# Kernel optimization log

Measured on AMD Instinct MI355X. Metric: run time of the kernel, lower is better.

Reference implementation:

```python
import jax, jax.numpy as jnp
import numpy as np

N = 50000      # nodes (full graph: num_dst == num_src == N)
E = 800000     # edges, avg degree 16
D = 128        # in_feats == n_hidden == out_feats
L = 3          # n_layers
EPS = 1e-5     # BatchNorm1d eps


def setup_inputs() -> dict:
    key = jax.random.key(0)
    ks = jax.random.split(key, 6)
    feat = jax.random.normal(ks[0], (N, D), dtype=jnp.float32)
    src = jax.random.randint(ks[1], (E,), 0, N)
    dst = jax.random.randint(ks[2], (E,), 0, N)
    scale = 1.0 / np.sqrt(D)
    W_self = jax.random.normal(ks[3], (L, D, D), dtype=jnp.float32) * scale
    W_neigh = jax.random.normal(ks[4], (L, D, D), dtype=jnp.float32) * scale
    b = jax.random.normal(ks[5], (L, D), dtype=jnp.float32) * 0.01
    gamma = jnp.ones((L - 1, D), dtype=jnp.float32)
    beta = jnp.zeros((L - 1, D), dtype=jnp.float32)
    return {"feat": feat, "src": src, "dst": dst, "W_self": W_self,
            "W_neigh": W_neigh, "b": b, "gamma": gamma, "beta": beta}


def reference(feat, src, dst, W_self, W_neigh, b, gamma, beta):
    n = feat.shape[0]
    n_layers = W_self.shape[0]
    # in-degree of each dst node, clamped to 1 (zero-degree nodes aggregate 0)
    deg = jax.ops.segment_sum(jnp.ones_like(dst, dtype=feat.dtype), dst,
                              num_segments=n)
    deg = jnp.maximum(deg, 1.0)[:, None]                      # [N,1]
    h = feat
    for i in range(n_layers):
        # mean aggregation over incoming neighbors: gather + segment-sum
        agg = jax.ops.segment_sum(h[src], dst, num_segments=n) / deg  # [N,D]
        # SAGEConv('mean'): fc_self(h_dst) + fc_neigh(agg) + bias
        hn = h @ W_self[i] + agg @ W_neigh[i] + b[i]
        hn = hn + h                                           # residual (dims match)
        if i < n_layers - 1:
            mu = jnp.mean(hn, axis=0)
            var = jnp.var(hn, axis=0)                         # biased, as BN training
            hn = (hn - mu) * jax.lax.rsqrt(var + EPS) * gamma[i] + beta[i]
            hn = jax.nn.relu(hn)
        h = hn
    return h
```

## Files before the change

kernel.cpp:

```cpp
#include <hip/hip_runtime.h>

#define DIM 128
#define EPSF 1e-5f
#define BK_SHIFT 10
#define BK_NODES 1024
#define BK_CAP 20480

typedef __attribute__((ext_vector_type(8))) short short8;
typedef __attribute__((ext_vector_type(8))) unsigned short ushort8;
typedef __attribute__((ext_vector_type(4))) float float4v;

__device__ inline unsigned short f2bf(float x) {
    union { float f; unsigned u; } z; z.f = x;
    unsigned u = z.u;
    unsigned r = u + 0x7FFF + ((u >> 16) & 1);
    return (unsigned short)(r >> 16);
}
__device__ inline float bf2f(unsigned short u) {
    union { unsigned u; float f; } z; z.u = ((unsigned)u) << 16;
    return z.f;
}

__global__ void binA_kernel(const int* __restrict__ src, const int* __restrict__ dst,
                            unsigned* __restrict__ barr, int* __restrict__ bcnt,
                            int E, int NB) {
    __shared__ int cnt[64];
    __shared__ int gcur[64];
    int tid = threadIdx.x;
    int tile0 = blockIdx.x * 4096;
    if (tid < 64) cnt[tid] = 0;
    __syncthreads();
    unsigned pk[16]; int bk[16];
#pragma unroll
    for (int i = 0; i < 16; ++i) {
        int e = tile0 + i * 256 + tid;
        if (e < E) {
            int d = dst[e];
            int s = src[e];
            bk[i] = d >> BK_SHIFT;
            pk[i] = ((unsigned)(d & (BK_NODES - 1)) << 16) | (unsigned)s;
            atomicAdd(&cnt[bk[i]], 1);
        } else bk[i] = -1;
    }
    __syncthreads();
    if (tid < 64) {
        int c = (tid < NB) ? cnt[tid] : 0;
        gcur[tid] = (c > 0) ? atomicAdd(&bcnt[tid], c) : 0;
    }
    __syncthreads();
#pragma unroll
    for (int i = 0; i < 16; ++i) {
        if (bk[i] >= 0) {
            int pos = atomicAdd(&gcur[bk[i]], 1);
            if (pos < BK_CAP)
                barr[(size_t)bk[i] * BK_CAP + pos] = pk[i];
        }
    }
}

__global__ void bucketscan_kernel(const int* __restrict__ bcnt, int* __restrict__ bbase,
                                  int NB, int* __restrict__ rowptr, int N, int E) {
    if (threadIdx.x == 0) {
        int run = 0;
        for (int b = 0; b < NB; ++b) { bbase[b] = run; run += bcnt[b]; }
        rowptr[N] = E;
    }
}

__global__ void binB_kernel(const unsigned* __restrict__ barr, const int* __restrict__ bcnt,
                            const int* __restrict__ bbase, int* __restrict__ rowptr,
                            int* __restrict__ colidx, int N) {
    __shared__ int hist[BK_NODES];
    __shared__ int sm[256];
    int b = blockIdx.x;
    int tid = threadIdx.x;
    int cnt = bcnt[b];
    if (cnt > BK_CAP) cnt = BK_CAP;
    const unsigned* arr = barr + (size_t)b * BK_CAP;
    int gb = bbase[b];
#pragma unroll
    for (int j = 0; j < 4; ++j) hist[tid * 4 + j] = 0;
    __syncthreads();
    for (int i = tid; i < cnt; i += 256)
        atomicAdd(&hist[arr[i] >> 16], 1);
    __syncthreads();
    int h[4], s = 0;
#pragma unroll
    for (int j = 0; j < 4; ++j) { h[j] = hist[tid * 4 + j]; s += h[j]; }
    sm[tid] = s;
    __syncthreads();
    int tot = s;
    for (int off = 1; off < 256; off <<= 1) {
        int x = (tid >= off) ? sm[tid - off] : 0;
        __syncthreads();
        sm[tid] += x;
        __syncthreads();
    }
    int run = sm[tid] - tot;
#pragma unroll
    for (int j = 0; j < 4; ++j) { hist[tid * 4 + j] = run; run += h[j]; }
    __syncthreads();
    int nbase = b << BK_SHIFT;
    int nn = N - nbase; if (nn > BK_NODES) nn = BK_NODES;
    for (int j = tid; j < nn; j += 256)
        rowptr[nbase + j] = gb + hist[j];
    __syncthreads();
    for (int i = tid; i < cnt; i += 256) {
        unsigned u = arr[i];
        int pos = atomicAdd(&hist[u >> 16], 1);
        colidx[gb + pos] = (int)(u & 0xFFFFu);
    }
}

__global__ void packw_kernel(const float* __restrict__ Ws, const float* __restrict__ Wn,
                             unsigned short* __restrict__ wpack) {
    int l = blockIdx.x >> 3;
    int s = blockIdx.x & 7;
    int tid = threadIdx.x;
#pragma unroll
    for (int pi = 0; pi < 2; ++pi) {
        int p = tid * 2 + pi;
        int nt = p >> 6;
        int lane = p & 63;
        int kb = s * 32 + (lane >> 4) * 8;
        int col = nt * 16 + (lane & 15);
        unsigned short* dstp = wpack + (size_t)l * 32768 + ((size_t)(s * 8 + nt) * 64 + lane) * 8;
#pragma unroll
        for (int j = 0; j < 8; ++j) {
            int k = kb + j;
            float v = (k < 128) ? Ws[(size_t)l * 16384 + k * 128 + col]
                                : Wn[(size_t)l * 16384 + (k - 128) * 128 + col];
            dstp[j] = f2bf(v);
        }
    }
}

__global__ void convert_kernel(const float* __restrict__ feat, unsigned short* __restrict__ Acat,
                               int N) {
    int idx = blockIdx.x * blockDim.x + threadIdx.x;
    if (idx >= N * 32) return;
    float4 v = ((const float4*)feat)[idx];
    int r = idx >> 5, c4 = idx & 31;
    ushort4 o;
    o.x = f2bf(v.x); o.y = f2bf(v.y); o.z = f2bf(v.z); o.w = f2bf(v.w);
    ((ushort4*)Acat)[(size_t)r * 64 + c4] = o;
}

__global__ void aggregate_kernel(unsigned short* Acat, const int* __restrict__ rowptr,
                                 const int* __restrict__ colidx, int N) {
    int wid = (blockIdx.x * blockDim.x + threadIdx.x) >> 6;
    if (wid >= N) return;
    int lane = threadIdx.x & 63;
    int half = lane >> 5, sl = lane & 31;
    int beg = rowptr[wid], end = rowptr[wid + 1];
    float4 acc = make_float4(0.f, 0.f, 0.f, 0.f);
    int e = beg + half;
    for (; e + 2 < end; e += 4) {
        int s0 = colidx[e];
        int s1 = colidx[e + 2];
        ushort4 u0 = *(const ushort4*)(Acat + (size_t)s0 * 256 + sl * 4);
        ushort4 u1 = *(const ushort4*)(Acat + (size_t)s1 * 256 + sl * 4);
        acc.x += bf2f(u0.x) + bf2f(u1.x);
        acc.y += bf2f(u0.y) + bf2f(u1.y);
        acc.z += bf2f(u0.z) + bf2f(u1.z);
        acc.w += bf2f(u0.w) + bf2f(u1.w);
    }
    if (e < end) {
        int s0 = colidx[e];
        ushort4 u0 = *(const ushort4*)(Acat + (size_t)s0 * 256 + sl * 4);
        acc.x += bf2f(u0.x);
        acc.y += bf2f(u0.y);
        acc.z += bf2f(u0.z);
        acc.w += bf2f(u0.w);
    }
    acc.x += __shfl_xor(acc.x, 32);
    acc.y += __shfl_xor(acc.y, 32);
    acc.z += __shfl_xor(acc.z, 32);
    acc.w += __shfl_xor(acc.w, 32);
    if (half == 0) {
        int deg = end - beg;
        float inv = 1.0f / (float)(deg > 0 ? deg : 1);
        ushort4 o;
        o.x = f2bf(acc.x * inv); o.y = f2bf(acc.y * inv);
        o.z = f2bf(acc.z * inv); o.w = f2bf(acc.w * inv);
        *(ushort4*)(Acat + (size_t)wid * 256 + 128 + sl * 4) = o;
    }
}

__launch_bounds__(256)
__global__ void gemm_kernel(const unsigned short* __restrict__ Acat,
                            const unsigned short* __restrict__ wpack,
                            const float* __restrict__ bias,
                            unsigned short* __restrict__ outb, float* __restrict__ outf,
                            float* __restrict__ stats, int withStats, int N) {
    __shared__ unsigned short Bs[32768];
    int tid = threadIdx.x;
    {
        const float4* wsrc = (const float4*)wpack;
        float4* bdst = (float4*)Bs;
#pragma unroll
        for (int i = 0; i < 16; ++i) bdst[i * 256 + tid] = wsrc[i * 256 + tid];
    }
    __syncthreads();

    int wave = tid >> 6, lane = tid & 63;
    int row0 = blockIdx.x * 128 + wave * 32;
    int mrow = lane & 15, kq = lane >> 4;
    const unsigned short* Abase = Acat + (size_t)(row0 + mrow) * 256 + kq * 8;

    float4v acc[2][8];
#pragma unroll
    for (int i = 0; i < 2; ++i)
#pragma unroll
        for (int j = 0; j < 8; ++j) acc[i][j] = (float4v){0.f, 0.f, 0.f, 0.f};

#pragma unroll
    for (int s = 0; s < 8; ++s) {
        short8 a0 = *(const short8*)(Abase + s * 32);
        short8 a1 = *(const short8*)(Abase + 16 * 256 + s * 32);
#pragma unroll
        for (int nt = 0; nt < 8; ++nt) {
            short8 b = *(const short8*)(Bs + ((size_t)(s * 8 + nt) * 64 + lane) * 8);
            acc[0][nt] = __builtin_amdgcn_mfma_f32_16x16x32_bf16(a0, b, acc[0][nt], 0, 0, 0);
            acc[1][nt] = __builtin_amdgcn_mfma_f32_16x16x32_bf16(a1, b, acc[1][nt], 0, 0, 0);
        }
    }

    float* sm = (float*)Bs;
    if (withStats) {
        __syncthreads();
        sm[tid] = 0.f;
        __syncthreads();
    }

    int colb = lane & 15;
    int rq = (lane >> 4) * 4;
#pragma unroll
    for (int mt = 0; mt < 2; ++mt) {
        int rowt = row0 + mt * 16 + rq;
#pragma unroll
        for (int nt = 0; nt < 8; ++nt) {
            int col = nt * 16 + colb;
            float bv = bias[col];
            float slo = 0.f, qlo = 0.f;
#pragma unroll
            for (int r = 0; r < 4; ++r) {
                int row = rowt + r;
                if (row < N) {
                    float res = bf2f(Acat[(size_t)row * 256 + col]);
                    float v = acc[mt][nt][r] + bv + res;
                    if (withStats) {
                        outb[(size_t)row * 128 + col] = f2bf(v);
                        slo += v; qlo += v * v;
                    } else {
                        outf[(size_t)row * 128 + col] = v;
                    }
                }
            }
            if (withStats) {
                atomicAdd(&sm[col], slo);
                atomicAdd(&sm[128 + col], qlo);
            }
        }
    }
    if (withStats) {
        __syncthreads();
        if (tid < 128) {
            atomicAdd(&stats[tid], sm[tid]);
            atomicAdd(&stats[128 + tid], sm[128 + tid]);
        }
    }
}

__global__ void bnapply_kernel(const unsigned short* __restrict__ hn,
                               unsigned short* __restrict__ Acat,
                               const float* __restrict__ stats, const float* __restrict__ gamma,
                               const float* __restrict__ beta, float invN, int N) {
    __shared__ float sc_s[128], sh_s[128];
    int tid = threadIdx.x;
    if (tid < 128) {
        float mean = stats[tid] * invN;
        float var = stats[128 + tid] * invN - mean * mean;
        float sc = gamma[tid] * rsqrtf(var + EPSF);
        sc_s[tid] = sc;
        sh_s[tid] = beta[tid] - mean * sc;
    }
    __syncthreads();
    int idx = blockIdx.x * 256 + tid;
    if (idx >= N * 32) return;
    int row = idx >> 5, c4 = idx & 31;
    ushort4 u = *(const ushort4*)(hn + (size_t)idx * 4);
    ushort4 o;
    {
        int col = c4 * 4;
        float v0 = fmaf(bf2f(u.x), sc_s[col], sh_s[col]);
        float v1 = fmaf(bf2f(u.y), sc_s[col + 1], sh_s[col + 1]);
        float v2 = fmaf(bf2f(u.z), sc_s[col + 2], sh_s[col + 2]);
        float v3 = fmaf(bf2f(u.w), sc_s[col + 3], sh_s[col + 3]);
        o.x = f2bf(fmaxf(v0, 0.f));
        o.y = f2bf(fmaxf(v1, 0.f));
        o.z = f2bf(fmaxf(v2, 0.f));
        o.w = f2bf(fmaxf(v3, 0.f));
    }
    *(ushort4*)(Acat + (size_t)row * 256 + c4 * 4) = o;
}

extern "C" void kernel_launch(void* const* d_in, const int* in_sizes, int n_in,
                              void* d_out, int out_size, void* d_ws, size_t ws_size,
                              hipStream_t stream) {
    const float* feat  = (const float*)d_in[0];
    const int*   src   = (const int*)d_in[1];
    const int*   dst   = (const int*)d_in[2];
    const float* Wself = (const float*)d_in[3];
    const float* Wneig = (const float*)d_in[4];
    const float* bias  = (const float*)d_in[5];
    const float* gamma = (const float*)d_in[6];
    const float* beta  = (const float*)d_in[7];

    int N = in_sizes[0] / DIM;
    int E = in_sizes[1];
    int Npad = (N + 127) & ~127;
    int NB = (N + BK_NODES - 1) >> BK_SHIFT;

    char* ws = (char*)d_ws;
    size_t off = 0;
    auto alloc = [&](size_t bytes) -> void* {
        void* p = ws + off;
        off = (off + bytes + 255) & ~(size_t)255;
        return p;
    };
    unsigned short* Acat   = (unsigned short*)alloc((size_t)Npad * 256 * 2);
    unsigned short* hnS    = (unsigned short*)alloc((size_t)Npad * 128 * 2);
    unsigned short* wpack  = (unsigned short*)alloc((size_t)3 * 32768 * 2);
    int*   colidx = (int*)alloc((size_t)E * 4);
    int*   rowptr = (int*)alloc((size_t)(N + 1) * 4);
    int*   bcnt   = (int*)alloc(64 * 4);
    int*   bbase  = (int*)alloc(64 * 4);
    float* stats  = (float*)alloc(256 * 4);

    unsigned* barr = (unsigned*)Acat;

    hipMemsetAsync(bcnt, 0, 64 * 4, stream);
    binA_kernel<<<(E + 4095) / 4096, 256, 0, stream>>>(src, dst, barr, bcnt, E, NB);
    bucketscan_kernel<<<1, 64, 0, stream>>>(bcnt, bbase, NB, rowptr, N, E);
    binB_kernel<<<NB, 256, 0, stream>>>(barr, bcnt, bbase, rowptr, colidx, N);

    packw_kernel<<<24, 256, 0, stream>>>(Wself, Wneig, wpack);
    convert_kernel<<<(N * 32 + 255) / 256, 256, 0, stream>>>(feat, Acat, N);
    if (Npad > N)
        hipMemsetAsync(Acat + (size_t)N * 256, 0, (size_t)(Npad - N) * 512, stream);

    float invN = 1.0f / (float)N;

    for (int l = 0; l < 3; ++l) {
        aggregate_kernel<<<(N + 3) / 4, 256, 0, stream>>>(Acat, rowptr, colidx, N);
        int withStats = (l < 2) ? 1 : 0;
        if (withStats) hipMemsetAsync(stats, 0, 256 * 4, stream);
        gemm_kernel<<<Npad / 128, 256, 0, stream>>>(
            Acat, wpack + (size_t)l * 32768, bias + (size_t)l * DIM,
            hnS, (float*)d_out, stats, withStats, N);
        if (withStats)
            bnapply_kernel<<<(N * 32 + 255) / 256, 256, 0, stream>>>(
                hnS, Acat, stats, gamma + (size_t)l * DIM, beta + (size_t)l * DIM, invN, N);
    }
}
```

Baseline: 364.5 us.

## Fold bucket scan into binB, zero stats in aggregate, use half-wave per node

Removes the single-thread bucketscan launch by having each binB block compute its own prefix from the bucket counts in shared memory. Removes the per-layer stats memset by zeroing the stats buffer from block 0 of the aggregate kernel. The aggregate kernel now assigns 32 lanes per node instead of a full 64-lane wave split into two halves, which doubles nodes per wave and drops the cross-half shuffle reduction. The cost is a longer serial edge loop per node and fewer loads in flight per node.

```diff
diff --git a/kernel.cpp b/kernel.cpp
--- a/kernel.cpp
+++ b/kernel.cpp
@@ -7,7 +7,6 @@
 #define BK_CAP 20480
 
 typedef __attribute__((ext_vector_type(8))) short short8;
-typedef __attribute__((ext_vector_type(8))) unsigned short ushort8;
 typedef __attribute__((ext_vector_type(4))) float float4v;
 
 __device__ inline unsigned short f2bf(float x) {
@@ -58,26 +57,28 @@
     }
 }
 
-__global__ void bucketscan_kernel(const int* __restrict__ bcnt, int* __restrict__ bbase,
-                                  int NB, int* __restrict__ rowptr, int N, int E) {
-    if (threadIdx.x == 0) {
-        int run = 0;
-        for (int b = 0; b < NB; ++b) { bbase[b] = run; run += bcnt[b]; }
-        rowptr[N] = E;
-    }
-}
-
 __global__ void binB_kernel(const unsigned* __restrict__ barr, const int* __restrict__ bcnt,
-                            const int* __restrict__ bbase, int* __restrict__ rowptr,
-                            int* __restrict__ colidx, int N) {
+                            int* __restrict__ rowptr, int* __restrict__ colidx,
+                            int N, int E, int NB) {
     __shared__ int hist[BK_NODES];
     __shared__ int sm[256];
+    __shared__ int bc[64];
+    __shared__ int gbS;
     int b = blockIdx.x;
     int tid = threadIdx.x;
-    int cnt = bcnt[b];
+    if (tid < 64) bc[tid] = (tid < NB) ? bcnt[tid] : 0;
+    __syncthreads();
+    if (tid == 0) {
+        int run = 0;
+        for (int i = 0; i < b; ++i) run += bc[i];
+        gbS = run;
+        if (b == 0) rowptr[N] = E;
+    }
+    __syncthreads();
+    int cnt = bc[b];
     if (cnt > BK_CAP) cnt = BK_CAP;
     const unsigned* arr = barr + (size_t)b * BK_CAP;
-    int gb = bbase[b];
+    int gb = gbS;
 #pragma unroll
     for (int j = 0; j < 4; ++j) hist[tid * 4 + j] = 0;
     __syncthreads();
@@ -147,17 +148,18 @@
 }
 
 __global__ void aggregate_kernel(unsigned short* Acat, const int* __restrict__ rowptr,
-                                 const int* __restrict__ colidx, int N) {
-    int wid = (blockIdx.x * blockDim.x + threadIdx.x) >> 6;
-    if (wid >= N) return;
-    int lane = threadIdx.x & 63;
-    int half = lane >> 5, sl = lane & 31;
-    int beg = rowptr[wid], end = rowptr[wid + 1];
+                                 const int* __restrict__ colidx, float* __restrict__ stats,
+                                 int N) {
+    if (blockIdx.x == 0) stats[threadIdx.x] = 0.f;
+    int node = (blockIdx.x * blockDim.x + threadIdx.x) >> 5;
+    if (node >= N) return;
+    int sl = threadIdx.x & 31;
+    int beg = rowptr[node], end = rowptr[node + 1];
     float4 acc = make_float4(0.f, 0.f, 0.f, 0.f);
-    int e = beg + half;
-    for (; e + 2 < end; e += 4) {
+    int e = beg;
+    for (; e + 1 < end; e += 2) {
         int s0 = colidx[e];
-        int s1 = colidx[e + 2];
+        int s1 = colidx[e + 1];
         ushort4 u0 = *(const ushort4*)(Acat + (size_t)s0 * 256 + sl * 4);
         ushort4 u1 = *(const ushort4*)(Acat + (size_t)s1 * 256 + sl * 4);
         acc.x += bf2f(u0.x) + bf2f(u1.x);
@@ -173,18 +175,12 @@
         acc.z += bf2f(u0.z);
         acc.w += bf2f(u0.w);
     }
-    acc.x += __shfl_xor(acc.x, 32);
-    acc.y += __shfl_xor(acc.y, 32);
-    acc.z += __shfl_xor(acc.z, 32);
-    acc.w += __shfl_xor(acc.w, 32);
-    if (half == 0) {
-        int deg = end - beg;
-        float inv = 1.0f / (float)(deg > 0 ? deg : 1);
-        ushort4 o;
-        o.x = f2bf(acc.x * inv); o.y = f2bf(acc.y * inv);
-        o.z = f2bf(acc.z * inv); o.w = f2bf(acc.w * inv);
-        *(ushort4*)(Acat + (size_t)wid * 256 + 128 + sl * 4) = o;
-    }
+    int deg = end - beg;
+    float inv = 1.0f / (float)(deg > 0 ? deg : 1);
+    ushort4 o;
+    o.x = f2bf(acc.x * inv); o.y = f2bf(acc.y * inv);
+    o.z = f2bf(acc.z * inv); o.w = f2bf(acc.w * inv);
+    *(ushort4*)(Acat + (size_t)node * 256 + 128 + sl * 4) = o;
 }
 
 __launch_bounds__(256)
@@ -335,15 +331,13 @@
     int*   colidx = (int*)alloc((size_t)E * 4);
     int*   rowptr = (int*)alloc((size_t)(N + 1) * 4);
     int*   bcnt   = (int*)alloc(64 * 4);
-    int*   bbase  = (int*)alloc(64 * 4);
     float* stats  = (float*)alloc(256 * 4);
 
     unsigned* barr = (unsigned*)Acat;
 
     hipMemsetAsync(bcnt, 0, 64 * 4, stream);
     binA_kernel<<<(E + 4095) / 4096, 256, 0, stream>>>(src, dst, barr, bcnt, E, NB);
-    bucketscan_kernel<<<1, 64, 0, stream>>>(bcnt, bbase, NB, rowptr, N, E);
-    binB_kernel<<<NB, 256, 0, stream>>>(barr, bcnt, bbase, rowptr, colidx, N);
+    binB_kernel<<<NB, 256, 0, stream>>>(barr, bcnt, rowptr, colidx, N, E, NB);
 
     packw_kernel<<<24, 256, 0, stream>>>(Wself, Wneig, wpack);
     convert_kernel<<<(N * 32 + 255) / 256, 256, 0, stream>>>(feat, Acat, N);
@@ -353,9 +347,8 @@
     float invN = 1.0f / (float)N;
 
     for (int l = 0; l < 3; ++l) {
-        aggregate_kernel<<<(N + 3) / 4, 256, 0, stream>>>(Acat, rowptr, colidx, N);
+        aggregate_kernel<<<(N * 32 + 255) / 256, 256, 0, stream>>>(Acat, rowptr, colidx, stats, N);
         int withStats = (l < 2) ? 1 : 0;
-        if (withStats) hipMemsetAsync(stats, 0, 256 * 4, stream);
         gemm_kernel<<<Npad / 128, 256, 0, stream>>>(
             Acat, wpack + (size_t)l * 32768, bias + (size_t)l * DIM,
             hnS, (float*)d_out, stats, withStats, N);
```

Result: slower. 384.5 us (+5.5%).
